# Optimization experiments

Measured on AMD Instinct MI355X. Metric: run time of the kernel, lower is better.

## Reference

```python
import jax, jax.numpy as jnp
import numpy as np

DT = 0.5
T_STEPS = int(2500 / DT)   # 5000
T_STIM = int(2000 / DT)    # 4000
A = 270.0; B_ = 108.0; D_ = 0.154; GAMMA = 0.641; TAU_S = 100.0; TAU_AMPA = 2.0
BATCH = 4096


def setup_inputs() -> dict:
    key = jax.random.key(0)
    k0, k1, k2, k3, k4 = jax.random.split(key, 5)
    return {
        "input_signal": jax.random.normal(k0, (BATCH, 1), dtype=jnp.float32),
        "J11": jnp.float32(0.2609), "J12": jnp.float32(0.0497),
        "J21": jnp.float32(0.0497), "J22": jnp.float32(0.2609),
        "J_ext": jnp.float32(0.0156), "I_0": jnp.float32(0.3255),
        "noise_ampa": jnp.float32(0.02), "threshold": jnp.float32(0.5),
        "motor_delay": jnp.float32(0.1),
        "eps0_1": jax.random.normal(k1, (BATCH, 1), dtype=jnp.float32),
        "eps0_2": jax.random.normal(k2, (BATCH, 1), dtype=jnp.float32),
        "eps_1": jax.random.normal(k3, (T_STEPS, BATCH, 1), dtype=jnp.float32),
        "eps_2": jax.random.normal(k4, (T_STEPS, BATCH, 1), dtype=jnp.float32),
    }


def _H(x):
    # Wong-Wang f-I curve: relu((a x - b) / (1 - exp(-d (a x - b)) + 1e-6))
    u = A * x - B_
    return jax.nn.relu(u / (1.0 - jnp.exp(-D_ * u) + 1e-6))


def _simulate(input_signal, J11, J12, J21, J22, J_ext, I_0, noise_ampa,
              eps0_1, eps0_2, eps_1, eps_2):
    decay = jnp.exp(jnp.float32(-DT / TAU_AMPA))
    nscale = jnp.float32(np.sqrt((1.0 - np.exp(-2.0 * DT / TAU_AMPA)) / 2.0))
    s0 = jnp.full_like(input_signal, 0.1)  # [B,1]
    carry0 = (s0, s0, eps0_1 * noise_ampa, eps0_2 * noise_ampa)

    def step(carry, xs):
        s1, s2, In1, In2 = carry
        e1, e2, t = xs
        stim = t < T_STIM
        I1 = jnp.where(stim, J_ext * (1.0 + input_signal / 100.0), 0.0)
        I2 = jnp.where(stim, J_ext * (1.0 - input_signal / 100.0), 0.0)
        x1 = J11 * s1 - J12 * s2 + I_0 + I1 + In1
        x2 = J22 * s2 - J21 * s1 + I_0 + I2 + In2
        ds1 = -(s1 / TAU_S) + (1.0 - s1) * _H(x1) * GAMMA / 1000.0
        ds2 = -(s2 / TAU_S) + (1.0 - s2) * _H(x2) * GAMMA / 1000.0
        In1n = In1 * decay + noise_ampa * nscale * e1
        In2n = In2 * decay + noise_ampa * nscale * e2
        s1n = s1 + ds1 * DT
        s2n = s2 + ds2 * DT
        ys = (jnp.concatenate([s1n, s2n], axis=-1),   # trajectory row [B,2]
              jnp.concatenate([ds1, ds2], axis=-1))   # dsdt row [B,2]
        return (s1n, s2n, In1n, In2n), ys

    ts = jnp.arange(T_STEPS)
    _, (traj, dsdt) = jax.lax.scan(step, carry0, (eps_1, eps_2, ts))
    return traj, dsdt  # each [T, B, 2]


def _decide(traj_m):
    # traj_m = trajectory - threshold; first-crossing times per unit
    m1 = traj_m[:, :, 0] > 0
    m2 = traj_m[:, :, 1] > 0
    inf = jnp.float32(jnp.inf)
    t1 = jnp.where(m1.any(0), jnp.argmax(m1, axis=0).astype(jnp.float32), inf)
    t2 = jnp.where(m2.any(0), jnp.argmax(m2, axis=0).astype(jnp.float32), inf)
    dtimes = jnp.where(t1 < t2, t1, -t2)
    return dtimes * DT


def reference(input_signal, J11, J12, J21, J22, J_ext, I_0, noise_ampa,
              threshold, motor_delay, eps0_1, eps0_2, eps_1, eps_2):
    traj, dsdt = _simulate(input_signal, J11, J12, J21, J22, J_ext, I_0,
                           noise_ampa, eps0_1, eps0_2, eps_1, eps_2)
    out = _decide(traj - threshold)  # [B], signed decision time in ms
    out = jnp.where(out < 0, out / 1000.0 - motor_delay,
                    jnp.where(out > 0, out / 1000.0 + motor_delay, out))
    return out
```

## Files before the change

kernel.cpp:

```cpp
#include <hip/hip_runtime.h>

#define BATCHN 4096
#define NSTEPS 5000
#define NSTIM  4000
#define U      25
#define NBLK      (NSTEPS / U)
#define NBLK_STIM (NSTIM / U)
#define ELPB   32

static __device__ __forceinline__ float swap_pair(float v) {
    return __int_as_float(
        __builtin_amdgcn_mov_dpp(__float_as_int(v), 0xB1, 0xF, 0xF, true));
}

__global__ __launch_bounds__(64, 1) void ww_kernel(
    const float* __restrict__ input_signal,
    const float* __restrict__ sJ11, const float* __restrict__ sJ12,
    const float* __restrict__ sJ21, const float* __restrict__ sJ22,
    const float* __restrict__ sJext, const float* __restrict__ sI0,
    const float* __restrict__ sNoise, const float* __restrict__ sThr,
    const float* __restrict__ sDelay,
    const float* __restrict__ eps0_1, const float* __restrict__ eps0_2,
    const float* __restrict__ eps_1, const float* __restrict__ eps_2,
    float* __restrict__ out)
{
    const int lane = threadIdx.x;
    const int unit = lane & 1;
    const int b    = blockIdx.x * ELPB + (lane >> 1);

    const float KE = -0.22217503629690245f;

    const float J11 = sJ11[0], J12 = sJ12[0], J21 = sJ21[0], J22 = sJ22[0];
    const float K270 = KE * 270.0f;
    const float B11 = K270 * J11, nB12 = -K270 * J12;
    const float B22 = K270 * J22, nB21 = -K270 * J21;
    const float Bs = unit ? B22 : B11;
    const float Bc = unit ? nB21 : nB12;
    const float nKE  = -KE;
    const float KE1p = 1.000001f * KE;
    const float SM = 0.995f;
    const float QC = 3.205e-4f;

    const float noise = sNoise[0];
    const float Jext = sJext[0], I0 = sI0[0];
    const float thr = sThr[0], delay = sDelay[0];

    const float inp = input_signal[b];
    const float Pself = unit
        ? fmaf(270.0f, I0 + Jext * (1.0f - inp * 0.01f), -108.0f)
        : fmaf(270.0f, I0 + Jext * (1.0f + inp * 0.01f), -108.0f);
    const float Pn  = fmaf(270.0f, I0, -108.0f);
    const float KPs = KE * Pself, KPn = KE * Pn;

    const float decay = 0.7788007830714049f;
    const float kKE   = KE * noise * 0.4435478165294536f * 270.0f;
    const float n270K = noise * 270.0f * KE;

    const float* __restrict__ ep = (unit ? eps_2 : eps_1) + b;
    float VK = (unit ? eps0_2[b] : eps0_1[b]) * n270K;

    float s = 0.1f;
    const float INF = __builtin_inff();
    float tm = INF;
    float tf = 0.0f;

    float bufA[U], bufB[U];

    auto loadE = [&](float (&buf)[U], int blk) {
        const size_t off = (size_t)blk * ((size_t)U * BATCHN);
        #pragma unroll
        for (int i = 0; i < U; ++i)
            buf[i] = ep[off + (size_t)i * BATCHN];
    };

    auto stepBlk = [&](const float (&buf)[U], int blk) -> bool {
        const float KP = (blk < NBLK_STIM) ? KPs : KPn;
        #pragma unroll
        for (int i = 0; i < U; ++i) {
            float kc = VK + KP;
            VK = fmaf(VK, decay, kKE * buf[i]);
            float sc = swap_pair(s);
            float w  = fmaf(Bs, s, fmaf(Bc, sc, kc));
            float x  = __builtin_amdgcn_exp2f(w);
            float r  = __builtin_amdgcn_rcpf(fmaf(nKE, x, KE1p));
            float h  = fmaxf(w * r, 0.0f);
            s = fmaf(h, fmaf(-QC, s, QC), SM * s);
            tm = fminf(tm, (s > thr) ? tf : INF);
            tf += 1.0f;
        }
        float pm = fminf(tm, swap_pair(tm));
        return __all(pm < INF);
    };

    loadE(bufA, 0);
    for (int blk = 0; blk < NBLK; blk += 2) {
        loadE(bufB, blk + 1);
        if (stepBlk(bufA, blk)) break;
        if (blk + 2 < NBLK) loadE(bufA, blk + 2);
        if (stepBlk(bufB, blk + 1)) break;
    }

    float to = swap_pair(tm);
    if (unit == 0) {
        float t1 = tm, t2 = to;
        float o;
        if (t1 == INF && t2 == INF) {
            o = -3.0e38f;
        } else {
            float dtm = (t1 < t2) ? t1 : -t2;
            o = dtm * 0.5f;
            if (o < 0.0f)      o = o / 1000.0f - delay;
            else if (o > 0.0f) o = o / 1000.0f + delay;
        }
        out[b] = o;
    }
}

extern "C" void kernel_launch(void* const* d_in, const int* in_sizes, int n_in,
                              void* d_out, int out_size, void* d_ws, size_t ws_size,
                              hipStream_t stream) {
    ww_kernel<<<dim3(BATCHN / ELPB), dim3(64), 0, stream>>>(
        (const float*)d_in[0],
        (const float*)d_in[1],
        (const float*)d_in[2],
        (const float*)d_in[3],
        (const float*)d_in[4],
        (const float*)d_in[5],
        (const float*)d_in[6],
        (const float*)d_in[7],
        (const float*)d_in[8],
        (const float*)d_in[9],
        (const float*)d_in[10],
        (const float*)d_in[11],
        (const float*)d_in[12],
        (const float*)d_in[13],
        (float*)d_out);
}
```

Baseline: 421.5 us.

## Process both populations per lane instead of pairing lanes via DPP swaps

Each lane now simulates one batch element, holding both units s1 and s2, instead of two lanes per element exchanging state through DPP swaps. The grid is halved to 64 blocks of 64 lanes. This removes the per-step cross-lane move and gives two independent dependency chains per lane for instruction-level parallelism. It also reformulates the relu update as max(z, sm) with the QC factor folded into an FMA. The cost is only 64 wavefronts on a 256-CU device, which lowers occupancy, roughly doubles register use for eps buffers, and makes the serial per-step chain longer.

```diff
diff --git a/kernel.cpp b/kernel.cpp
--- a/kernel.cpp
+++ b/kernel.cpp
@@ -6,12 +6,7 @@
 #define U      25
 #define NBLK      (NSTEPS / U)
 #define NBLK_STIM (NSTIM / U)
-#define ELPB   32
-
-static __device__ __forceinline__ float swap_pair(float v) {
-    return __int_as_float(
-        __builtin_amdgcn_mov_dpp(__float_as_int(v), 0xB1, 0xF, 0xF, true));
-}
+#define ELPB   64
 
 __global__ __launch_bounds__(64, 1) void ww_kernel(
     const float* __restrict__ input_signal,
@@ -25,8 +20,7 @@
     float* __restrict__ out)
 {
     const int lane = threadIdx.x;
-    const int unit = lane & 1;
-    const int b    = blockIdx.x * ELPB + (lane >> 1);
+    const int b    = blockIdx.x * ELPB + lane;
 
     const float KE = -0.22217503629690245f;
 
@@ -34,8 +28,6 @@
     const float K270 = KE * 270.0f;
     const float B11 = K270 * J11, nB12 = -K270 * J12;
     const float B22 = K270 * J22, nB21 = -K270 * J21;
-    const float Bs = unit ? B22 : B11;
-    const float Bc = unit ? nB21 : nB12;
     const float nKE  = -KE;
     const float KE1p = 1.000001f * KE;
     const float SM = 0.995f;
@@ -46,74 +38,90 @@
     const float thr = sThr[0], delay = sDelay[0];
 
     const float inp = input_signal[b];
-    const float Pself = unit
-        ? fmaf(270.0f, I0 + Jext * (1.0f - inp * 0.01f), -108.0f)
-        : fmaf(270.0f, I0 + Jext * (1.0f + inp * 0.01f), -108.0f);
-    const float Pn  = fmaf(270.0f, I0, -108.0f);
-    const float KPs = KE * Pself, KPn = KE * Pn;
+    const float P1 = fmaf(270.0f, I0 + Jext * (1.0f + inp * 0.01f), -108.0f);
+    const float P2 = fmaf(270.0f, I0 + Jext * (1.0f - inp * 0.01f), -108.0f);
+    const float Pn = fmaf(270.0f, I0, -108.0f);
+    const float KP1s = KE * P1, KP2s = KE * P2, KPn = KE * Pn;
 
     const float decay = 0.7788007830714049f;
     const float kKE   = KE * noise * 0.4435478165294536f * 270.0f;
     const float n270K = noise * 270.0f * KE;
 
-    const float* __restrict__ ep = (unit ? eps_2 : eps_1) + b;
-    float VK = (unit ? eps0_2[b] : eps0_1[b]) * n270K;
+    const float* __restrict__ ep1 = eps_1 + b;
+    const float* __restrict__ ep2 = eps_2 + b;
+    float VK1 = eps0_1[b] * n270K;
+    float VK2 = eps0_2[b] * n270K;
 
-    float s = 0.1f;
+    float s1 = 0.1f, s2 = 0.1f;
     const float INF = __builtin_inff();
-    float tm = INF;
+    float tm1 = INF, tm2 = INF;
     float tf = 0.0f;
 
-    float bufA[U], bufB[U];
+    float bufA1[U], bufA2[U], bufB1[U], bufB2[U];
 
-    auto loadE = [&](float (&buf)[U], int blk) {
+    auto loadE = [&](float (&b1)[U], float (&b2)[U], int blk) {
         const size_t off = (size_t)blk * ((size_t)U * BATCHN);
         #pragma unroll
-        for (int i = 0; i < U; ++i)
-            buf[i] = ep[off + (size_t)i * BATCHN];
+        for (int i = 0; i < U; ++i) {
+            b1[i] = ep1[off + (size_t)i * BATCHN];
+            b2[i] = ep2[off + (size_t)i * BATCHN];
+        }
     };
 
-    auto stepBlk = [&](const float (&buf)[U], int blk) -> bool {
-        const float KP = (blk < NBLK_STIM) ? KPs : KPn;
+    auto stepBlk = [&](const float (&e1)[U], const float (&e2)[U],
+                       int blk) -> bool {
+        const bool stim = (blk < NBLK_STIM);
+        const float KP1 = stim ? KP1s : KPn;
+        const float KP2 = stim ? KP2s : KPn;
         #pragma unroll
         for (int i = 0; i < U; ++i) {
-            float kc = VK + KP;
-            VK = fmaf(VK, decay, kKE * buf[i]);
-            float sc = swap_pair(s);
-            float w  = fmaf(Bs, s, fmaf(Bc, sc, kc));
-            float x  = __builtin_amdgcn_exp2f(w);
-            float r  = __builtin_amdgcn_rcpf(fmaf(nKE, x, KE1p));
-            float h  = fmaxf(w * r, 0.0f);
-            s = fmaf(h, fmaf(-QC, s, QC), SM * s);
-            tm = fminf(tm, (s > thr) ? tf : INF);
+            float kc1 = VK1 + KP1;
+            float kc2 = VK2 + KP2;
+            VK1 = fmaf(VK1, decay, kKE * e1[i]);
+            VK2 = fmaf(VK2, decay, kKE * e2[i]);
+            float w1 = fmaf(B11, s1, fmaf(nB12, s2, kc1));
+            float w2 = fmaf(B22, s2, fmaf(nB21, s1, kc2));
+            float x1 = __builtin_amdgcn_exp2f(w1);
+            float x2 = __builtin_amdgcn_exp2f(w2);
+            float q1  = fmaf(-QC, s1, QC);
+            float q2  = fmaf(-QC, s2, QC);
+            float sm1 = SM * s1;
+            float sm2 = SM * s2;
+            float qw1 = q1 * w1;
+            float qw2 = q2 * w2;
+            float d1 = fmaf(nKE, x1, KE1p);
+            float d2 = fmaf(nKE, x2, KE1p);
+            float r1 = __builtin_amdgcn_rcpf(d1);
+            float r2 = __builtin_amdgcn_rcpf(d2);
+            float z1 = fmaf(qw1, r1, sm1);
+            float z2 = fmaf(qw2, r2, sm2);
+            s1 = fmaxf(z1, sm1);
+            s2 = fmaxf(z2, sm2);
+            tm1 = fminf(tm1, (s1 > thr) ? tf : INF);
+            tm2 = fminf(tm2, (s2 > thr) ? tf : INF);
             tf += 1.0f;
         }
-        float pm = fminf(tm, swap_pair(tm));
-        return __all(pm < INF);
+        return __all(fminf(tm1, tm2) < INF);
     };
 
-    loadE(bufA, 0);
+    loadE(bufA1, bufA2, 0);
     for (int blk = 0; blk < NBLK; blk += 2) {
-        loadE(bufB, blk + 1);
-        if (stepBlk(bufA, blk)) break;
-        if (blk + 2 < NBLK) loadE(bufA, blk + 2);
-        if (stepBlk(bufB, blk + 1)) break;
+        loadE(bufB1, bufB2, blk + 1);
+        if (stepBlk(bufA1, bufA2, blk)) break;
+        if (blk + 2 < NBLK) loadE(bufA1, bufA2, blk + 2);
+        if (stepBlk(bufB1, bufB2, blk + 1)) break;
     }
 
-    float to = swap_pair(tm);
-    if (unit == 0) {
-        float t1 = tm, t2 = to;
-        float o;
-        if (t1 == INF && t2 == INF) {
-            o = -3.0e38f;
-        } else {
-            float dtm = (t1 < t2) ? t1 : -t2;
-            o = dtm * 0.5f;
-            if (o < 0.0f)      o = o / 1000.0f - delay;
-            else if (o > 0.0f) o = o / 1000.0f + delay;
-        }
-        out[b] = o;
+    float o;
+    if (tm1 == INF && tm2 == INF) {
+        o = -3.0e38f;
+    } else {
+        float dtm = (tm1 < tm2) ? tm1 : -tm2;
+        o = dtm * 0.5f;
+        if (o < 0.0f)      o = o / 1000.0f - delay;
+        else if (o > 0.0f) o = o / 1000.0f + delay;
     }
+    out[b] = o;
 }
 
 extern "C" void kernel_launch(void* const* d_in, const int* in_sizes, int n_in,
```

Measured after the change: 585.9 us. 1.39x slower.
